# Optimization experiments

Hardware: AMD Instinct MI355X
Metric: run time of the kernel (lower is better)

The kernel has to match this reference:

```python
import jax, jax.numpy as jnp
import numpy as np

N_NODES = 100000
N_EDGES = 640000
H_FEATS = 128


def setup_inputs() -> dict:
    key = jax.random.key(0)
    k_h, k_src, k_dst, k_w1, k_b1, k_w2, k_b2 = jax.random.split(key, 7)
    h = jax.random.normal(k_h, (N_NODES, H_FEATS), dtype=jnp.float32)
    src = jax.random.randint(k_src, (N_EDGES,), 0, N_NODES, dtype=jnp.int64)
    dst = jax.random.randint(k_dst, (N_EDGES,), 0, N_NODES, dtype=jnp.int64)
    # nn.Linear params: W1 (h_feats, 2*h_feats) as (out, in); store transposed for x @ W
    lim1 = 1.0 / np.sqrt(2 * H_FEATS)
    W1 = jax.random.uniform(k_w1, (2 * H_FEATS, H_FEATS), jnp.float32, -lim1, lim1)
    b1 = jax.random.uniform(k_b1, (H_FEATS,), jnp.float32, -lim1, lim1)
    lim2 = 1.0 / np.sqrt(H_FEATS)
    W2 = jax.random.uniform(k_w2, (H_FEATS, 1), jnp.float32, -lim2, lim2)
    b2 = jax.random.uniform(k_b2, (1,), jnp.float32, -lim2, lim2)
    return {"h": h, "src": src, "dst": dst, "W1": W1, "b1": b1, "W2": W2, "b2": b2}


def reference(h, src, dst, W1, b1, W2, b2):
    # gather src/dst node features per edge and concat: [E, 2*h_feats]
    he = jnp.concatenate([h[src], h[dst]], axis=1)
    hidden = jax.nn.relu(he @ W1 + b1)          # [E, h_feats]
    score = (hidden @ W2 + b2)[:, 0]            # [E]
    return score
```

## Files before the change

kernel.cpp:

```cpp
#include <hip/hip_runtime.h>

#define N_NODES 100000
#define N_EDGES 640000
#define F 128
#define NT 6250
#define NBLK 512
#define EBLK 2500

typedef __attribute__((ext_vector_type(8))) short short8;
typedef __attribute__((ext_vector_type(4))) float float4v;

static __device__ __forceinline__ unsigned short f2bf(float f) {
    unsigned int u = __float_as_uint(f);
    u += 0x7fffu + ((u >> 16) & 1u);
    return (unsigned short)(u >> 16);
}

__global__ __launch_bounds__(256) void prep_wt(
    const float* __restrict__ W1, unsigned short* __restrict__ Wt)
{
    int id = blockIdx.x * 256 + threadIdx.x;
    int n = id >> 7, k = id & 127;
    float v = W1[((n & 128) + k) * 128 + (n & 127)];
    Wt[id] = f2bf(v);
}

__global__ __launch_bounds__(256, 2) void node_proj(
    const float* __restrict__ h, const unsigned short* __restrict__ Wt,
    const float* __restrict__ b1,
    unsigned short* __restrict__ A, unsigned short* __restrict__ B)
{
    __shared__ unsigned short w_swz[256 * 128];
    __shared__ unsigned short hb[16 * 136];
    __shared__ unsigned short oA[16 * 136];
    __shared__ unsigned short oB[16 * 136];

    const int tid  = threadIdx.x;
    const int lane = tid & 63;
    const int l16  = lane & 15;
    const int quad = lane >> 4;
    const int w    = tid >> 6;

#pragma unroll
    for (int i = 0; i < 16; ++i) {
        int cl = i * 256 + tid;
        int r = cl >> 4, c = cl & 15;
        uint4 v = *(const uint4*)(Wt + (size_t)r * F + c * 8);
        *(uint4*)&w_swz[((r << 4) + (c ^ (r & 15))) * 8] = v;
    }

    const bool isA = (w < 2);
    const int colb = (w & 1) * 64;
    float4 bv[4];
#pragma unroll
    for (int p = 0; p < 4; ++p) {
        int col = colb + p * 16 + quad * 4;
        bv[p] = isA ? *(const float4*)(b1 + col) : make_float4(0.f, 0.f, 0.f, 0.f);
    }
    unsigned short* ostage = isA ? oA : oB;

    int srow[2], sc4[2];
#pragma unroll
    for (int i = 0; i < 2; ++i) { int f = i * 256 + tid; srow[i] = f >> 5; sc4[i] = f & 31; }

#define LOADH(PF, T)                                                           \
    _Pragma("unroll") for (int i = 0; i < 2; ++i)                              \
        PF[i] = *(const float4*)(h + ((size_t)(T) * 16 + srow[i]) * F + sc4[i] * 4);

#define CVTWRITE(PF)                                                           \
    _Pragma("unroll") for (int i = 0; i < 2; ++i) {                            \
        uint2 p;                                                               \
        p.x = (unsigned)f2bf(PF[i].x) | ((unsigned)f2bf(PF[i].y) << 16);       \
        p.y = (unsigned)f2bf(PF[i].z) | ((unsigned)f2bf(PF[i].w) << 16);       \
        *(uint2*)&hb[srow[i] * 136 + sc4[i] * 4] = p;                          \
    }

    int t = blockIdx.x;
    float4 pfA[2], pfB[2];
    LOADH(pfA, t); CVTWRITE(pfA);
    LOADH(pfA, t + NBLK);
    __syncthreads();

    while (t < NT) {
        const int tn  = t + NBLK;
        const int tnn = tn + NBLK;
        if (tnn < NT) LOADH(pfB, tnn);

        float4v acc[4];
#pragma unroll
        for (int p = 0; p < 4; ++p) acc[p] = (float4v){0.f, 0.f, 0.f, 0.f};
#pragma unroll
        for (int k0 = 0; k0 < 4; ++k0) {
            short8 bf = *(const short8*)&hb[l16 * 136 + k0 * 32 + quad * 8];
            const int cc = (k0 * 4 + quad);
#pragma unroll
            for (int p = 0; p < 4; ++p) {
                const int row = w * 64 + p * 16 + l16;
                short8 af = *(const short8*)&w_swz[((row << 4) + (cc ^ l16)) * 8];
                acc[p] = __builtin_amdgcn_mfma_f32_16x16x32_bf16(af, bf, acc[p], 0, 0, 0);
            }
        }
        __syncthreads();

        if (tn < NT) CVTWRITE(pfA);
#pragma unroll
        for (int p = 0; p < 4; ++p) {
            ushort4 sv;
            sv.x = f2bf(acc[p][0] + bv[p].x);
            sv.y = f2bf(acc[p][1] + bv[p].y);
            sv.z = f2bf(acc[p][2] + bv[p].z);
            sv.w = f2bf(acc[p][3] + bv[p].w);
            *(ushort4*)&ostage[l16 * 136 + colb + p * 16 + quad * 4] = sv;
        }
        __syncthreads();

        {
            const int r = tid >> 4, c = tid & 15;
            const size_t goff = ((size_t)t * 16 + r) * F + c * 8;
            *(uint4*)(A + goff) = *(const uint4*)&oA[r * 136 + c * 8];
            *(uint4*)(B + goff) = *(const uint4*)&oB[r * 136 + c * 8];
        }

#pragma unroll
        for (int i = 0; i < 2; ++i) pfA[i] = pfB[i];
        t = tn;
    }
#undef LOADH
#undef CVTWRITE
}

__global__ __launch_bounds__(256) void edge_score(
    const unsigned short* __restrict__ A, const unsigned short* __restrict__ B,
    const int* __restrict__ src, const int* __restrict__ dst,
    const float* __restrict__ W2, const float* __restrict__ b2,
    float* __restrict__ out)
{
    const int tid = threadIdx.x;
    const int sub = tid & 7;
    const int e0  = blockIdx.x * 256 + (tid >> 3) * 4;
    const int e1  = e0 + 128;

    const int4 sv0 = *(const int4*)(src + e0);
    const int4 dv0 = *(const int4*)(dst + e0);
    const int4 sv1 = *(const int4*)(src + e1);
    const int4 dv1 = *(const int4*)(dst + e1);
    const int s0[4] = {sv0.x, sv0.y, sv0.z, sv0.w};
    const int d0[4] = {dv0.x, dv0.y, dv0.z, dv0.w};
    const int s1[4] = {sv1.x, sv1.y, sv1.z, sv1.w};
    const int d1[4] = {dv1.x, dv1.y, dv1.z, dv1.w};

    uint4 a00[4], a01[4], b00[4], b01[4];
    uint4 a10[4], a11[4], b10[4], b11[4];
#pragma unroll
    for (int i = 0; i < 4; ++i) {
        const unsigned short* Ar = A + (size_t)s0[i] * F;
        const unsigned short* Br = B + (size_t)d0[i] * F;
        a00[i] = *(const uint4*)(Ar + sub * 8);
        a01[i] = *(const uint4*)(Ar + 64 + sub * 8);
        b00[i] = *(const uint4*)(Br + sub * 8);
        b01[i] = *(const uint4*)(Br + 64 + sub * 8);
    }
#pragma unroll
    for (int i = 0; i < 4; ++i) {
        const unsigned short* Ar = A + (size_t)s1[i] * F;
        const unsigned short* Br = B + (size_t)d1[i] * F;
        a10[i] = *(const uint4*)(Ar + sub * 8);
        a11[i] = *(const uint4*)(Ar + 64 + sub * 8);
        b10[i] = *(const uint4*)(Br + sub * 8);
        b11[i] = *(const uint4*)(Br + 64 + sub * 8);
    }

    const float4 w0 = *(const float4*)(W2 + sub * 8);
    const float4 w1 = *(const float4*)(W2 + sub * 8 + 4);
    const float4 w2 = *(const float4*)(W2 + 64 + sub * 8);
    const float4 w3 = *(const float4*)(W2 + 64 + sub * 8 + 4);
    const float bias = b2[0];

#define TERM(UA, UB, WL, WH)                                                   \
    {                                                                          \
        float fa0 = __uint_as_float((UA) << 16);                               \
        float fa1 = __uint_as_float((UA) & 0xFFFF0000u);                       \
        float fb0 = __uint_as_float((UB) << 16);                               \
        float fb1 = __uint_as_float((UB) & 0xFFFF0000u);                       \
        sacc = fmaf(fmaxf(fa0 + fb0, 0.f), (WL), sacc);                        \
        sacc = fmaf(fmaxf(fa1 + fb1, 0.f), (WH), sacc);                        \
    }
#define BATCH(AV0, AV1, BV0, BV1, EBASE)                                       \
    _Pragma("unroll")                                                          \
    for (int i = 0; i < 4; ++i) {                                              \
        float sacc = 0.f;                                                      \
        TERM(AV0[i].x, BV0[i].x, w0.x, w0.y)                                   \
        TERM(AV0[i].y, BV0[i].y, w0.z, w0.w)                                   \
        TERM(AV0[i].z, BV0[i].z, w1.x, w1.y)                                   \
        TERM(AV0[i].w, BV0[i].w, w1.z, w1.w)                                   \
        TERM(AV1[i].x, BV1[i].x, w2.x, w2.y)                                   \
        TERM(AV1[i].y, BV1[i].y, w2.z, w2.w)                                   \
        TERM(AV1[i].z, BV1[i].z, w3.x, w3.y)                                   \
        TERM(AV1[i].w, BV1[i].w, w3.z, w3.w)                                   \
        sacc += __shfl_xor(sacc, 1);                                           \
        sacc += __shfl_xor(sacc, 2);                                           \
        sacc += __shfl_xor(sacc, 4);                                           \
        if (sub == 0) out[(EBASE) + i] = sacc + bias;                          \
    }

    BATCH(a00, a01, b00, b01, e0)
    BATCH(a10, a11, b10, b11, e1)
#undef BATCH
#undef TERM
}

extern "C" void kernel_launch(void* const* d_in, const int* in_sizes, int n_in,
                              void* d_out, int out_size, void* d_ws, size_t ws_size,
                              hipStream_t stream) {
    const float* h   = (const float*)d_in[0];
    const int*   src = (const int*)d_in[1];
    const int*   dst = (const int*)d_in[2];
    const float* W1  = (const float*)d_in[3];
    const float* b1  = (const float*)d_in[4];
    const float* W2  = (const float*)d_in[5];
    const float* b2  = (const float*)d_in[6];
    float* out = (float*)d_out;

    unsigned short* Wt = (unsigned short*)d_ws;
    unsigned short* A  = Wt + 256 * 128;
    unsigned short* B  = A + (size_t)N_NODES * F;

    prep_wt<<<128, 256, 0, stream>>>(W1, Wt);
    node_proj<<<NBLK, 256, 0, stream>>>(h, Wt, b1, A, B);
    edge_score<<<EBLK, 256, 0, stream>>>(A, B, src, dst, W2, b2, out);
}
```

Before: 152.8 us.

## Quantize per-node projections to int8 with per-row scales for edge gather

The node projection kernel now stores the A and B intermediates as int8 with one float scale per node row, instead of bf16. The scale comes from a per-row max-abs reduction done with shuffles. The edge kernel gathers half as many bytes per edge plus two scales, then dequantizes before the ReLU and dot product. This targets the random-gather bandwidth of the edge stage. The cost is lower precision in the intermediates and some extra quantize and dequantize arithmetic.

```diff
diff --git a/kernel.cpp b/kernel.cpp
--- a/kernel.cpp
+++ b/kernel.cpp
@@ -28,7 +28,8 @@
 __global__ __launch_bounds__(256, 2) void node_proj(
     const float* __restrict__ h, const unsigned short* __restrict__ Wt,
     const float* __restrict__ b1,
-    unsigned short* __restrict__ A, unsigned short* __restrict__ B)
+    unsigned char* __restrict__ A8, unsigned char* __restrict__ B8,
+    float* __restrict__ sA, float* __restrict__ sB)
 {
     __shared__ unsigned short w_swz[256 * 128];
     __shared__ unsigned short hb[16 * 136];
@@ -116,9 +117,45 @@
 
         {
             const int r = tid >> 4, c = tid & 15;
-            const size_t goff = ((size_t)t * 16 + r) * F + c * 8;
-            *(uint4*)(A + goff) = *(const uint4*)&oA[r * 136 + c * 8];
-            *(uint4*)(B + goff) = *(const uint4*)&oB[r * 136 + c * 8];
+            const int node = t * 16 + r;
+            uint4 va = *(const uint4*)&oA[r * 136 + c * 8];
+            uint4 vb = *(const uint4*)&oB[r * 136 + c * 8];
+            float fa[8], fb[8];
+#define UNPK(W, F0, F1)                                                        \
+            F0 = __uint_as_float((W) << 16);                                   \
+            F1 = __uint_as_float((W) & 0xFFFF0000u);
+            UNPK(va.x, fa[0], fa[1]) UNPK(va.y, fa[2], fa[3])
+            UNPK(va.z, fa[4], fa[5]) UNPK(va.w, fa[6], fa[7])
+            UNPK(vb.x, fb[0], fb[1]) UNPK(vb.y, fb[2], fb[3])
+            UNPK(vb.z, fb[4], fb[5]) UNPK(vb.w, fb[6], fb[7])
+#undef UNPK
+            float ma = 0.f, mb = 0.f;
+#pragma unroll
+            for (int j = 0; j < 8; ++j) {
+                ma = fmaxf(ma, fabsf(fa[j]));
+                mb = fmaxf(mb, fabsf(fb[j]));
+            }
+#pragma unroll
+            for (int m = 1; m < 16; m <<= 1) {
+                ma = fmaxf(ma, __shfl_xor(ma, m));
+                mb = fmaxf(mb, __shfl_xor(mb, m));
+            }
+            const float inva = ma > 0.f ? 127.f / ma : 0.f;
+            const float invb = mb > 0.f ? 127.f / mb : 0.f;
+            uint2 qa, qb; qa.x = qa.y = qb.x = qb.y = 0u;
+#pragma unroll
+            for (int j = 0; j < 4; ++j) {
+                qa.x |= ((unsigned)((int)rintf(fa[j] * inva) & 255)) << (8 * j);
+                qa.y |= ((unsigned)((int)rintf(fa[j + 4] * inva) & 255)) << (8 * j);
+                qb.x |= ((unsigned)((int)rintf(fb[j] * invb) & 255)) << (8 * j);
+                qb.y |= ((unsigned)((int)rintf(fb[j + 4] * invb) & 255)) << (8 * j);
+            }
+            *(uint2*)(A8 + (size_t)node * 128 + c * 8) = qa;
+            *(uint2*)(B8 + (size_t)node * 128 + c * 8) = qb;
+            if (c == 0) {
+                sA[node] = ma * (1.f / 127.f);
+                sB[node] = mb * (1.f / 127.f);
+            }
         }
 
 #pragma unroll
@@ -129,8 +166,23 @@
 #undef CVTWRITE
 }
 
+static __device__ __forceinline__ float dot4q(
+    unsigned ua, unsigned ub, float sa, float sb, float4 wv, float acc)
+{
+    const float* wp = &wv.x;
+#pragma unroll
+    for (int j = 0; j < 4; ++j) {
+        float fa = (float)((int)(signed char)(ua >> (8 * j)));
+        float fb = (float)((int)(signed char)(ub >> (8 * j)));
+        float hv = fmaf(fa, sa, fb * sb);
+        acc = fmaf(fmaxf(hv, 0.f), wp[j], acc);
+    }
+    return acc;
+}
+
 __global__ __launch_bounds__(256) void edge_score(
-    const unsigned short* __restrict__ A, const unsigned short* __restrict__ B,
+    const unsigned char* __restrict__ A8, const unsigned char* __restrict__ B8,
+    const float* __restrict__ sA, const float* __restrict__ sB,
     const int* __restrict__ src, const int* __restrict__ dst,
     const float* __restrict__ W2, const float* __restrict__ b2,
     float* __restrict__ out)
@@ -149,25 +201,30 @@
     const int s1[4] = {sv1.x, sv1.y, sv1.z, sv1.w};
     const int d1[4] = {dv1.x, dv1.y, dv1.z, dv1.w};
 
-    uint4 a00[4], a01[4], b00[4], b01[4];
-    uint4 a10[4], a11[4], b10[4], b11[4];
+    uint2 a00[4], a01[4], b00[4], b01[4];
+    uint2 a10[4], a11[4], b10[4], b11[4];
+    float sa0[4], sb0[4], sa1[4], sb1[4];
 #pragma unroll
     for (int i = 0; i < 4; ++i) {
-        const unsigned short* Ar = A + (size_t)s0[i] * F;
-        const unsigned short* Br = B + (size_t)d0[i] * F;
-        a00[i] = *(const uint4*)(Ar + sub * 8);
-        a01[i] = *(const uint4*)(Ar + 64 + sub * 8);
-        b00[i] = *(const uint4*)(Br + sub * 8);
-        b01[i] = *(const uint4*)(Br + 64 + sub * 8);
+        const unsigned char* Ar = A8 + (size_t)s0[i] * 128;
+        const unsigned char* Br = B8 + (size_t)d0[i] * 128;
+        a00[i] = *(const uint2*)(Ar + sub * 8);
+        a01[i] = *(const uint2*)(Ar + 64 + sub * 8);
+        b00[i] = *(const uint2*)(Br + sub * 8);
+        b01[i] = *(const uint2*)(Br + 64 + sub * 8);
+        sa0[i] = sA[s0[i]];
+        sb0[i] = sB[d0[i]];
     }
 #pragma unroll
     for (int i = 0; i < 4; ++i) {
-        const unsigned short* Ar = A + (size_t)s1[i] * F;
-        const unsigned short* Br = B + (size_t)d1[i] * F;
-        a10[i] = *(const uint4*)(Ar + sub * 8);
-        a11[i] = *(const uint4*)(Ar + 64 + sub * 8);
-        b10[i] = *(const uint4*)(Br + sub * 8);
-        b11[i] = *(const uint4*)(Br + 64 + sub * 8);
+        const unsigned char* Ar = A8 + (size_t)s1[i] * 128;
+        const unsigned char* Br = B8 + (size_t)d1[i] * 128;
+        a10[i] = *(const uint2*)(Ar + sub * 8);
+        a11[i] = *(const uint2*)(Ar + 64 + sub * 8);
+        b10[i] = *(const uint2*)(Br + sub * 8);
+        b11[i] = *(const uint2*)(Br + 64 + sub * 8);
+        sa1[i] = sA[s1[i]];
+        sb1[i] = sB[d1[i]];
     }
 
     const float4 w0 = *(const float4*)(W2 + sub * 8);
@@ -176,37 +233,23 @@
     const float4 w3 = *(const float4*)(W2 + 64 + sub * 8 + 4);
     const float bias = b2[0];
 
-#define TERM(UA, UB, WL, WH)                                                   \
-    {                                                                          \
-        float fa0 = __uint_as_float((UA) << 16);                               \
-        float fa1 = __uint_as_float((UA) & 0xFFFF0000u);                       \
-        float fb0 = __uint_as_float((UB) << 16);                               \
-        float fb1 = __uint_as_float((UB) & 0xFFFF0000u);                       \
-        sacc = fmaf(fmaxf(fa0 + fb0, 0.f), (WL), sacc);                        \
-        sacc = fmaf(fmaxf(fa1 + fb1, 0.f), (WH), sacc);                        \
-    }
-#define BATCH(AV0, AV1, BV0, BV1, EBASE)                                       \
+#define BATCH(AV0, AV1, BV0, BV1, SAV, SBV, EBASE)                             \
     _Pragma("unroll")                                                          \
     for (int i = 0; i < 4; ++i) {                                              \
         float sacc = 0.f;                                                      \
-        TERM(AV0[i].x, BV0[i].x, w0.x, w0.y)                                   \
-        TERM(AV0[i].y, BV0[i].y, w0.z, w0.w)                                   \
-        TERM(AV0[i].z, BV0[i].z, w1.x, w1.y)                                   \
-        TERM(AV0[i].w, BV0[i].w, w1.z, w1.w)                                   \
-        TERM(AV1[i].x, BV1[i].x, w2.x, w2.y)                                   \
-        TERM(AV1[i].y, BV1[i].y, w2.z, w2.w)                                   \
-        TERM(AV1[i].z, BV1[i].z, w3.x, w3.y)                                   \
-        TERM(AV1[i].w, BV1[i].w, w3.z, w3.w)                                   \
+        sacc = dot4q(AV0[i].x, BV0[i].x, SAV[i], SBV[i], w0, sacc);            \
+        sacc = dot4q(AV0[i].y, BV0[i].y, SAV[i], SBV[i], w1, sacc);            \
+        sacc = dot4q(AV1[i].x, BV1[i].x, SAV[i], SBV[i], w2, sacc);            \
+        sacc = dot4q(AV1[i].y, BV1[i].y, SAV[i], SBV[i], w3, sacc);            \
         sacc += __shfl_xor(sacc, 1);                                           \
         sacc += __shfl_xor(sacc, 2);                                           \
         sacc += __shfl_xor(sacc, 4);                                           \
         if (sub == 0) out[(EBASE) + i] = sacc + bias;                          \
     }
 
-    BATCH(a00, a01, b00, b01, e0)
-    BATCH(a10, a11, b10, b11, e1)
+    BATCH(a00, a01, b00, b01, sa0, sb0, e0)
+    BATCH(a10, a11, b10, b11, sa1, sb1, e1)
 #undef BATCH
-#undef TERM
 }
 
 extern "C" void kernel_launch(void* const* d_in, const int* in_sizes, int n_in,
@@ -222,10 +265,12 @@
     float* out = (float*)d_out;
 
     unsigned short* Wt = (unsigned short*)d_ws;
-    unsigned short* A  = Wt + 256 * 128;
-    unsigned short* B  = A + (size_t)N_NODES * F;
+    unsigned char*  A8 = (unsigned char*)(Wt + 256 * 128);
+    unsigned char*  B8 = A8 + (size_t)N_NODES * 128;
+    float*          sA = (float*)(B8 + (size_t)N_NODES * 128);
+    float*          sB = sA + N_NODES;
 
     prep_wt<<<128, 256, 0, stream>>>(W1, Wt);
-    node_proj<<<NBLK, 256, 0, stream>>>(h, Wt, b1, A, B);
-    edge_score<<<EBLK, 256, 0, stream>>>(A, B, src, dst, W2, b2, out);
-}
+    node_proj<<<NBLK, 256, 0, stream>>>(h, Wt, b1, A8, B8, sA, sB);
+    edge_score<<<EBLK, 256, 0, stream>>>(A8, B8, sA, sB, src, dst, W2, b2, out);
+}
```

Result: faster. 139.6 us (-8.6%).
